# Kernel optimization log

Measured on AMD Instinct MI355X. Metric: run time of the kernel, lower is better.

The kernel has to match this reference:

```python
import jax, jax.numpy as jnp
import numpy as np

N = 200000          # number of points (dental scan vertices)
K = 16              # neighbors after dropping self (nsample=17 - 1)
C = 32              # feature dim (base_fdim)
NUM_CLASSES = 17
TEMPERATURE = 0.1
WEIGHT = 0.1        # head_cfg.weight[1:] of '.1'
EPS = 1e-8


def setup_inputs() -> dict:
    key = jax.random.key(0)
    k1, k2, k3 = jax.random.split(key, 3)
    features = jax.random.normal(k1, (N, C), dtype=jnp.float32)
    labels = jax.random.randint(k2, (N,), 0, NUM_CLASSES, dtype=jnp.int32)
    neighbor_idx = jax.random.randint(k3, (N, K), 0, N, dtype=jnp.int64)
    return {"features": features, "labels": labels, "neighbor_idx": neighbor_idx}


def reference(features, labels, neighbor_idx):
    # gather neighbor features/labels: [N, K, C] / [N, K]
    nb_feat = features[neighbor_idx]
    nb_lab = labels[neighbor_idx]

    # posmask_cnt: same class as center point (labels are argmaxed one-hots)
    posmask = nb_lab == labels[:, None]                     # [N, K] bool

    # point_mask: points with at least one positive and one negative neighbor
    cnt = jnp.sum(posmask.astype(jnp.int32), axis=-1)       # [N]
    point_mask = jnp.logical_and(cnt > 0, cnt < K)          # [N] bool

    # dist_l2
    diff = features[:, None, :] - nb_feat                   # [N, K, C]
    dist = jnp.sqrt(jnp.sum(diff * diff, axis=-1) + EPS)    # [N, K]

    # contrast_softnn (stable softmax over neighbors)
    d = -dist
    d = (d - jnp.max(d, axis=-1, keepdims=True)) / TEMPERATURE
    e = jnp.exp(d)                                          # [N, K]
    pos = jnp.sum(e * posmask.astype(e.dtype), axis=-1)
    neg = jnp.sum(e, axis=-1)
    loss = -jnp.log(pos / neg + EPS)                        # [N]

    # masked mean over valid points (== filtering before the mean)
    pm = point_mask.astype(loss.dtype)
    denom = jnp.maximum(jnp.sum(pm), 1.0)
    mean_loss = jnp.sum(loss * pm) / denom
    return mean_loss * WEIGHT
```

## Files before the change

kernel.cpp:

```cpp
#include <hip/hip_runtime.h>
#include <math.h>
#include <string.h>

#define NPTS 200000
#define KNBR 16
#define CDIM 32
#define NITEM (NPTS * KNBR)
#define TEMP 0.1f
#define WEIGHT 0.1f
#define EPSV 1e-8f

#define PART_BLOCKS 2048
#define CHUNK (NITEM / 1024)
#define BLD_BLOCKS ((NPTS + 255) / 256)

#define SMP_BLOCKS 625
#define SMP_STRIDE (SMP_BLOCKS * 256)
#define SMP_ITER (NITEM / SMP_STRIDE)

#define QS 0.55f

#define TBLA_OFF 256
#define TBLB_OFF (TBLA_OFF + NPTS * 16)
#define D2A_OFF  (TBLB_OFF + NPTS * 16)
#define D2B_OFF  (D2A_OFF + NITEM * 2)
#define BL_OFF   (D2B_OFF + NITEM * 2)
#define BC_OFF   (BL_OFF + SMP_BLOCKS * 4)
#define WS_NEEDED ((size_t)(BC_OFF + SMP_BLOCKS * 4))

typedef float v2f __attribute__((ext_vector_type(2)));

static __device__ __forceinline__ unsigned short f32_to_f16b(float x) {
    _Float16 h = (_Float16)x;
    unsigned short u;
    __builtin_memcpy(&u, &h, 2);
    return u;
}
static __device__ __forceinline__ float f16b_to_f32(unsigned short u) {
    _Float16 h;
    __builtin_memcpy(&h, &u, 2);
    return (float)h;
}
static __device__ __forceinline__ int q4(float x) {
    int q = (int)rintf(x * (1.0f / QS)) + 7;
    return q < 0 ? 0 : (q > 14 ? 14 : q);
}

__global__ __launch_bounds__(256) void build_tables(
    const float* __restrict__ f, const int* __restrict__ labels,
    unsigned char* __restrict__ A, unsigned char* __restrict__ B) {
    const int p = blockIdx.x * 256 + threadIdx.x;
    if (p >= NPTS) return;
    const float4* fp = (const float4*)(f + (size_t)p * CDIM);
    const float4 v0 = fp[0], v1 = fp[1], v2 = fp[2], v3 = fp[3];
    const float4 v4 = fp[4], v5 = fp[5], v6 = fp[6], v7 = fp[7];

    int a0 = 0, a1 = 0, a2 = 0, a3 = 0;
    a0 = __builtin_amdgcn_cvt_pk_fp8_f32(v0.x, v0.y, a0, false);
    a0 = __builtin_amdgcn_cvt_pk_fp8_f32(v0.z, v0.w, a0, true);
    a1 = __builtin_amdgcn_cvt_pk_fp8_f32(v1.x, v1.y, a1, false);
    a1 = __builtin_amdgcn_cvt_pk_fp8_f32(v1.z, v1.w, a1, true);
    a2 = __builtin_amdgcn_cvt_pk_fp8_f32(v2.x, v2.y, a2, false);
    a2 = __builtin_amdgcn_cvt_pk_fp8_f32(v2.z, v2.w, a2, true);
    a3 = __builtin_amdgcn_cvt_pk_fp8_f32(v3.x, v3.y, a3, false);
    a3 = __builtin_amdgcn_cvt_pk_fp8_f32(v3.z, v3.w, a3, true);
    uint4 ra; ra.x = a0; ra.y = a1; ra.z = a2; ra.w = a3;
    *(uint4*)(A + (size_t)p * 16) = ra;

    int b0 = 0, b1 = 0, b2 = 0, b3 = 0;
    b0 = __builtin_amdgcn_cvt_pk_fp8_f32(v4.x, v4.y, b0, false);
    b0 = __builtin_amdgcn_cvt_pk_fp8_f32(v4.z, v4.w, b0, true);
    b1 = __builtin_amdgcn_cvt_pk_fp8_f32(v5.x, v5.y, b1, false);
    b1 = __builtin_amdgcn_cvt_pk_fp8_f32(v5.z, v5.w, b1, true);
    b2 = __builtin_amdgcn_cvt_pk_fp8_f32(v6.x, v6.y, b2, false);
    b2 = __builtin_amdgcn_cvt_pk_fp8_f32(v6.z, v6.w, b2, true);
    b3 = __builtin_amdgcn_cvt_pk_fp8_f32(v7.x, v7.y, b3, false);
    const int pk = q4(v7.z) | (q4(v7.w) << 4);
    b3 = (b3 & 0xffff) | (pk << 16) | ((labels[p] & 0xff) << 24);
    uint4 rb; rb.x = b0; rb.y = b1; rb.z = b2; rb.w = b3;
    *(uint4*)(B + (size_t)p * 16) = rb;
}

__global__ __launch_bounds__(256) void partial_d2(
    const unsigned char* __restrict__ tblA,
    const unsigned char* __restrict__ tblB,
    const int* __restrict__ nbr,
    unsigned short* __restrict__ d2A,
    unsigned short* __restrict__ d2B) {
    const int b = blockIdx.x;
    const int grp = (b >> 2) & 1;
    const int r = (b >> 3) * 4 + (b & 3);
    const int i0 = r * CHUNK;

    if (grp == 0) {
        for (int t = threadIdx.x; t < CHUNK; t += 256) {
            const int i = i0 + t;
            const int idx = nbr[i];
            const int p = i >> 4;
            const uint4 nv = *(const uint4*)(tblA + (size_t)idx * 16);
            const uint4 cv = *(const uint4*)(tblA + (size_t)p * 16);
            const unsigned* pn = (const unsigned*)&nv;
            const unsigned* pc = (const unsigned*)&cv;
            float d2 = 0.f;
            #pragma unroll
            for (int q = 0; q < 4; ++q) {
                v2f nl = __builtin_amdgcn_cvt_pk_f32_fp8((int)pn[q], false);
                v2f nh = __builtin_amdgcn_cvt_pk_f32_fp8((int)pn[q], true);
                v2f cl = __builtin_amdgcn_cvt_pk_f32_fp8((int)pc[q], false);
                v2f ch = __builtin_amdgcn_cvt_pk_f32_fp8((int)pc[q], true);
                float a0 = cl.x - nl.x, a1 = cl.y - nl.y;
                float a2 = ch.x - nh.x, a3 = ch.y - nh.y;
                d2 += a0 * a0 + a1 * a1 + a2 * a2 + a3 * a3;
            }
            d2A[i] = f32_to_f16b(d2);
        }
    } else {
        for (int t = threadIdx.x; t < CHUNK; t += 256) {
            const int i = i0 + t;
            const int idx = nbr[i];
            const int p = i >> 4;
            const uint4 nv = *(const uint4*)(tblB + (size_t)idx * 16);
            const uint4 cv = *(const uint4*)(tblB + (size_t)p * 16);
            const unsigned* pn = (const unsigned*)&nv;
            const unsigned* pc = (const unsigned*)&cv;
            float d2 = 0.f;
            #pragma unroll
            for (int q = 0; q < 3; ++q) {
                v2f nl = __builtin_amdgcn_cvt_pk_f32_fp8((int)pn[q], false);
                v2f nh = __builtin_amdgcn_cvt_pk_f32_fp8((int)pn[q], true);
                v2f cl = __builtin_amdgcn_cvt_pk_f32_fp8((int)pc[q], false);
                v2f ch = __builtin_amdgcn_cvt_pk_f32_fp8((int)pc[q], true);
                float a0 = cl.x - nl.x, a1 = cl.y - nl.y;
                float a2 = ch.x - nh.x, a3 = ch.y - nh.y;
                d2 += a0 * a0 + a1 * a1 + a2 * a2 + a3 * a3;
            }
            {
                v2f nl = __builtin_amdgcn_cvt_pk_f32_fp8((int)pn[3], false);
                v2f cl = __builtin_amdgcn_cvt_pk_f32_fp8((int)pc[3], false);
                float a0 = cl.x - nl.x, a1 = cl.y - nl.y;
                d2 += a0 * a0 + a1 * a1;
            }
            {
                const unsigned nb = (pn[3] >> 16) & 0xffu;
                const unsigned cb = (pc[3] >> 16) & 0xffu;
                const float n30 = (float)(nb & 15u) * QS - 7.0f * QS;
                const float n31 = (float)(nb >> 4) * QS - 7.0f * QS;
                const float c30 = (float)(cb & 15u) * QS - 7.0f * QS;
                const float c31 = (float)(cb >> 4) * QS - 7.0f * QS;
                const float a0 = c30 - n30, a1 = c31 - n31;
                d2 += a0 * a0 + a1 * a1;
            }
            const bool pos = (pn[3] >> 24) == (pc[3] >> 24);
            d2B[i] = (unsigned short)(f32_to_f16b(d2) | (pos ? 0x8000u : 0u));
        }
    }
}

__global__ __launch_bounds__(256) void softmax_part(
    const unsigned short* __restrict__ d2A,
    const unsigned short* __restrict__ d2B,
    float* __restrict__ bl, float* __restrict__ bc) {
    const int tid = threadIdx.x;
    const int lane = tid & 63;
    float loss_acc = 0.f, valid_acc = 0.f;

    for (int k = 0; k < SMP_ITER; ++k) {
        const int i = blockIdx.x * 256 + tid + k * SMP_STRIDE;
        const unsigned short ua = d2A[i];
        const unsigned short ub = d2B[i];
        const bool pos = (ub & 0x8000u) != 0;
        const float d2v = f16b_to_f32(ua) + f16b_to_f32(ub & 0x7fffu);
        const float d = sqrtf(d2v + EPSV);

        float mn = d;
        mn = fminf(mn, __shfl_xor(mn, 1));
        mn = fminf(mn, __shfl_xor(mn, 2));
        mn = fminf(mn, __shfl_xor(mn, 4));
        mn = fminf(mn, __shfl_xor(mn, 8));
        const float e = expf((mn - d) * (1.0f / TEMP));

        float pos_s = pos ? e : 0.f;
        float neg_s = e;
        float cnt_s = pos ? 1.f : 0.f;
        #pragma unroll
        for (int off = 1; off <= 8; off <<= 1) {
            pos_s += __shfl_xor(pos_s, off);
            neg_s += __shfl_xor(neg_s, off);
            cnt_s += __shfl_xor(cnt_s, off);
        }
        if ((lane & 15) == 0) {
            const int icnt = (int)(cnt_s + 0.5f);
            if (icnt > 0 && icnt < KNBR) {
                loss_acc += -logf(pos_s / neg_s + EPSV);
                valid_acc += 1.f;
            }
        }
    }

    loss_acc += __shfl_xor(loss_acc, 16);
    valid_acc += __shfl_xor(valid_acc, 16);
    loss_acc += __shfl_xor(loss_acc, 32);
    valid_acc += __shfl_xor(valid_acc, 32);

    __shared__ float sl[4], sv[4];
    if (lane == 0) { sl[tid >> 6] = loss_acc; sv[tid >> 6] = valid_acc; }
    __syncthreads();
    if (tid == 0) {
        bl[blockIdx.x] = sl[0] + sl[1] + sl[2] + sl[3];
        bc[blockIdx.x] = sv[0] + sv[1] + sv[2] + sv[3];
    }
}

__global__ __launch_bounds__(256) void final_reduce(const float* __restrict__ bl,
                                                    const float* __restrict__ bc,
                                                    float* __restrict__ out) {
    const int tid = threadIdx.x;
    float l = 0.f, v = 0.f;
    for (int i = tid; i < SMP_BLOCKS; i += 256) { l += bl[i]; v += bc[i]; }
    #pragma unroll
    for (int off = 1; off <= 32; off <<= 1) {
        l += __shfl_xor(l, off);
        v += __shfl_xor(v, off);
    }
    __shared__ float sl[4], sv[4];
    if ((tid & 63) == 0) { sl[tid >> 6] = l; sv[tid >> 6] = v; }
    __syncthreads();
    if (tid == 0) {
        const float S = sl[0] + sl[1] + sl[2] + sl[3];
        const float C = sv[0] + sv[1] + sv[2] + sv[3];
        out[0] = S / fmaxf(C, 1.f) * WEIGHT;
    }
}

__global__ __launch_bounds__(256) void contrast_fp32(
    const float* __restrict__ features,
    const int* __restrict__ labels,
    const int* __restrict__ nbr,
    float* __restrict__ ws) {
    const int lane = threadIdx.x & 63;
    const int wave = threadIdx.x >> 6;
    const int p0 = blockIdx.x * 16 + wave * 4;
    const int m = lane >> 3;
    const int c = lane & 7;
    const int idx_l = nbr[p0 * KNBR + lane];
    const int labn_l = labels[idx_l];
    const int labc_l = labels[p0 + (lane >> 4)];
    float4 cen[4];
    #pragma unroll
    for (int pt = 0; pt < 4; ++pt)
        cen[pt] = *(const float4*)(features + (size_t)(p0 + pt) * CDIM + c * 4);
    int ridx[8];
    #pragma unroll
    for (int j = 0; j < 8; ++j) ridx[j] = __shfl(idx_l, 8 * j + m);
    float4 v[8];
    #pragma unroll
    for (int j = 0; j < 8; ++j)
        v[j] = *(const float4*)(features + (size_t)ridx[j] * CDIM + c * 4);
    float dj[8];
    #pragma unroll
    for (int j = 0; j < 8; ++j) {
        float4 ce = cen[j >> 1];
        float dx = ce.x - v[j].x, dy = ce.y - v[j].y;
        float dz = ce.z - v[j].z, dw = ce.w - v[j].w;
        float d2 = dx * dx + dy * dy + dz * dz + dw * dw;
        d2 += __shfl_xor(d2, 1);
        d2 += __shfl_xor(d2, 2);
        d2 += __shfl_xor(d2, 4);
        dj[j] = sqrtf(d2 + EPSV);
    }
    float loss_acc = 0.f, valid_acc = 0.f;
    #pragma unroll
    for (int pt = 0; pt < 4; ++pt) {
        float a = dj[2 * pt], b = dj[2 * pt + 1];
        float mn = fminf(a, b);
        mn = fminf(mn, __shfl_xor(mn, 8));
        mn = fminf(mn, __shfl_xor(mn, 16));
        mn = fminf(mn, __shfl_xor(mn, 32));
        const float ea = expf((mn - a) / TEMP);
        const float eb = expf((mn - b) / TEMP);
        const int la = __shfl(labn_l, 16 * pt + m);
        const int lb = __shfl(labn_l, 16 * pt + 8 + m);
        const int lc = __shfl(labc_l, 16 * pt);
        float pos_s = (la == lc ? ea : 0.f) + (lb == lc ? eb : 0.f);
        float neg_s = ea + eb;
        float cnt_s = (la == lc ? 1.f : 0.f) + (lb == lc ? 1.f : 0.f);
        #pragma unroll
        for (int off = 8; off <= 32; off <<= 1) {
            pos_s += __shfl_xor(pos_s, off);
            neg_s += __shfl_xor(neg_s, off);
            cnt_s += __shfl_xor(cnt_s, off);
        }
        if (lane == pt) {
            const int icnt = (int)(cnt_s + 0.5f);
            if (icnt > 0 && icnt < KNBR) {
                loss_acc += -logf(pos_s / neg_s + EPSV);
                valid_acc += 1.f;
            }
        }
    }
    __shared__ float s_loss, s_cnt;
    if (threadIdx.x == 0) { s_loss = 0.f; s_cnt = 0.f; }
    __syncthreads();
    if (lane < 4) { atomicAdd(&s_loss, loss_acc); atomicAdd(&s_cnt, valid_acc); }
    __syncthreads();
    if (threadIdx.x == 0) { atomicAdd(&ws[0], s_loss); atomicAdd(&ws[1], s_cnt); }
}

__global__ void contrast_finalize(const float* __restrict__ ws,
                                  float* __restrict__ out) {
    out[0] = ws[0] / fmaxf(ws[1], 1.f) * WEIGHT;
}

extern "C" void kernel_launch(void* const* d_in, const int* in_sizes, int n_in,
                              void* d_out, int out_size, void* d_ws, size_t ws_size,
                              hipStream_t stream) {
    const float* features = (const float*)d_in[0];
    const int* labels     = (const int*)d_in[1];
    const int* nbr        = (const int*)d_in[2];
    float* out = (float*)d_out;
    float* ws  = (float*)d_ws;

    if (ws_size >= WS_NEEDED) {
        unsigned char* tblA = (unsigned char*)d_ws + TBLA_OFF;
        unsigned char* tblB = (unsigned char*)d_ws + TBLB_OFF;
        unsigned short* d2A = (unsigned short*)((char*)d_ws + D2A_OFF);
        unsigned short* d2B = (unsigned short*)((char*)d_ws + D2B_OFF);
        float* bl = (float*)((char*)d_ws + BL_OFF);
        float* bc = (float*)((char*)d_ws + BC_OFF);

        build_tables<<<BLD_BLOCKS, 256, 0, stream>>>(features, labels, tblA, tblB);
        partial_d2<<<PART_BLOCKS, 256, 0, stream>>>(tblA, tblB, nbr, d2A, d2B);
        softmax_part<<<SMP_BLOCKS, 256, 0, stream>>>(d2A, d2B, bl, bc);
        final_reduce<<<1, 256, 0, stream>>>(bl, bc, out);
    } else {
        hipMemsetAsync(ws, 0, 16, stream);
        contrast_fp32<<<NPTS / 16, 256, 0, stream>>>(features, labels, nbr, ws);
        contrast_finalize<<<1, 1, 0, stream>>>(ws, out);
    }
}
```

Baseline: 138.0 us.

## Process four neighbors per thread with vectorized loads and nontemporal hints

The pairwise-distance kernel now gives each thread four consecutive neighbor entries of one point. It loads the four indices as one vector, loads and decodes the center row once, and stores the four fp16 results as a single 8-byte nontemporal write. The softmax kernel likewise reads four entries per thread, cutting the per-point shuffle reductions from 16 lanes to 4. Nontemporal loads are added for the streamed feature, index and intermediate buffers. This trades lower load instruction count, fewer shuffles and less redundant center decoding for more registers per thread and a grid-stride loop in place of fixed chunks.

```diff
diff --git a/kernel.cpp b/kernel.cpp
--- a/kernel.cpp
+++ b/kernel.cpp
@@ -10,13 +10,15 @@
 #define WEIGHT 0.1f
 #define EPSV 1e-8f
 
-#define PART_BLOCKS 2048
-#define CHUNK (NITEM / 1024)
 #define BLD_BLOCKS ((NPTS + 255) / 256)
 
+#define PD_BLOCKS 1248
+#define PD_RANKS 3125
+#define PD_GSTRIDE 624
+
 #define SMP_BLOCKS 625
-#define SMP_STRIDE (SMP_BLOCKS * 256)
-#define SMP_ITER (NITEM / SMP_STRIDE)
+#define SMP_ITER 5
+#define SMP_STRIDE (SMP_BLOCKS * 1024)
 
 #define QS 0.55f
 
@@ -29,6 +31,10 @@
 #define WS_NEEDED ((size_t)(BC_OFF + SMP_BLOCKS * 4))
 
 typedef float v2f __attribute__((ext_vector_type(2)));
+typedef float v4f __attribute__((ext_vector_type(4)));
+typedef int   v4i __attribute__((ext_vector_type(4)));
+typedef unsigned v4u __attribute__((ext_vector_type(4)));
+typedef unsigned v2u __attribute__((ext_vector_type(2)));
 
 static __device__ __forceinline__ unsigned short f32_to_f16b(float x) {
     _Float16 h = (_Float16)x;
@@ -51,9 +57,15 @@
     unsigned char* __restrict__ A, unsigned char* __restrict__ B) {
     const int p = blockIdx.x * 256 + threadIdx.x;
     if (p >= NPTS) return;
-    const float4* fp = (const float4*)(f + (size_t)p * CDIM);
-    const float4 v0 = fp[0], v1 = fp[1], v2 = fp[2], v3 = fp[3];
-    const float4 v4 = fp[4], v5 = fp[5], v6 = fp[6], v7 = fp[7];
+    const v4f* fp = (const v4f*)(f + (size_t)p * CDIM);
+    const v4f v0 = __builtin_nontemporal_load(fp + 0);
+    const v4f v1 = __builtin_nontemporal_load(fp + 1);
+    const v4f v2 = __builtin_nontemporal_load(fp + 2);
+    const v4f v3 = __builtin_nontemporal_load(fp + 3);
+    const v4f v4 = __builtin_nontemporal_load(fp + 4);
+    const v4f v5 = __builtin_nontemporal_load(fp + 5);
+    const v4f v6 = __builtin_nontemporal_load(fp + 6);
+    const v4f v7 = __builtin_nontemporal_load(fp + 7);
 
     int a0 = 0, a1 = 0, a2 = 0, a3 = 0;
     a0 = __builtin_amdgcn_cvt_pk_fp8_f32(v0.x, v0.y, a0, false);
@@ -64,8 +76,9 @@
     a2 = __builtin_amdgcn_cvt_pk_fp8_f32(v2.z, v2.w, a2, true);
     a3 = __builtin_amdgcn_cvt_pk_fp8_f32(v3.x, v3.y, a3, false);
     a3 = __builtin_amdgcn_cvt_pk_fp8_f32(v3.z, v3.w, a3, true);
-    uint4 ra; ra.x = a0; ra.y = a1; ra.z = a2; ra.w = a3;
-    *(uint4*)(A + (size_t)p * 16) = ra;
+    v4u ra; ra.x = (unsigned)a0; ra.y = (unsigned)a1;
+    ra.z = (unsigned)a2; ra.w = (unsigned)a3;
+    *(v4u*)(A + (size_t)p * 16) = ra;
 
     int b0 = 0, b1 = 0, b2 = 0, b3 = 0;
     b0 = __builtin_amdgcn_cvt_pk_fp8_f32(v4.x, v4.y, b0, false);
@@ -77,8 +90,9 @@
     b3 = __builtin_amdgcn_cvt_pk_fp8_f32(v7.x, v7.y, b3, false);
     const int pk = q4(v7.z) | (q4(v7.w) << 4);
     b3 = (b3 & 0xffff) | (pk << 16) | ((labels[p] & 0xff) << 24);
-    uint4 rb; rb.x = b0; rb.y = b1; rb.z = b2; rb.w = b3;
-    *(uint4*)(B + (size_t)p * 16) = rb;
+    v4u rb; rb.x = (unsigned)b0; rb.y = (unsigned)b1;
+    rb.z = (unsigned)b2; rb.w = (unsigned)b3;
+    *(v4u*)(B + (size_t)p * 16) = rb;
 }
 
 __global__ __launch_bounds__(256) void partial_d2(
@@ -90,69 +104,85 @@
     const int b = blockIdx.x;
     const int grp = (b >> 2) & 1;
     const int r = (b >> 3) * 4 + (b & 3);
-    const int i0 = r * CHUNK;
-
-    if (grp == 0) {
-        for (int t = threadIdx.x; t < CHUNK; t += 256) {
-            const int i = i0 + t;
-            const int idx = nbr[i];
-            const int p = i >> 4;
-            const uint4 nv = *(const uint4*)(tblA + (size_t)idx * 16);
-            const uint4 cv = *(const uint4*)(tblA + (size_t)p * 16);
-            const unsigned* pn = (const unsigned*)&nv;
-            const unsigned* pc = (const unsigned*)&cv;
-            float d2 = 0.f;
+    const unsigned char* __restrict__ tbl = grp ? tblB : tblA;
+    unsigned short* __restrict__ dst = grp ? d2B : d2A;
+
+    for (int rr = r; rr < PD_RANKS; rr += PD_GSTRIDE) {
+        const int i = rr * 1024 + threadIdx.x * 4;
+        const v4i idx4 = __builtin_nontemporal_load((const v4i*)(nbr + i));
+        const int p = i >> 4;
+        const v4u cv = *(const v4u*)(tbl + (size_t)p * 16);
+
+        v4u nv[4];
+        nv[0] = *(const v4u*)(tbl + (size_t)idx4.x * 16);
+        nv[1] = *(const v4u*)(tbl + (size_t)idx4.y * 16);
+        nv[2] = *(const v4u*)(tbl + (size_t)idx4.z * 16);
+        nv[3] = *(const v4u*)(tbl + (size_t)idx4.w * 16);
+
+        unsigned short o[4];
+        if (grp == 0) {
+            v2f c[8];
             #pragma unroll
             for (int q = 0; q < 4; ++q) {
-                v2f nl = __builtin_amdgcn_cvt_pk_f32_fp8((int)pn[q], false);
-                v2f nh = __builtin_amdgcn_cvt_pk_f32_fp8((int)pn[q], true);
-                v2f cl = __builtin_amdgcn_cvt_pk_f32_fp8((int)pc[q], false);
-                v2f ch = __builtin_amdgcn_cvt_pk_f32_fp8((int)pc[q], true);
-                float a0 = cl.x - nl.x, a1 = cl.y - nl.y;
-                float a2 = ch.x - nh.x, a3 = ch.y - nh.y;
-                d2 += a0 * a0 + a1 * a1 + a2 * a2 + a3 * a3;
-            }
-            d2A[i] = f32_to_f16b(d2);
-        }
-    } else {
-        for (int t = threadIdx.x; t < CHUNK; t += 256) {
-            const int i = i0 + t;
-            const int idx = nbr[i];
-            const int p = i >> 4;
-            const uint4 nv = *(const uint4*)(tblB + (size_t)idx * 16);
-            const uint4 cv = *(const uint4*)(tblB + (size_t)p * 16);
-            const unsigned* pn = (const unsigned*)&nv;
-            const unsigned* pc = (const unsigned*)&cv;
-            float d2 = 0.f;
+                c[2 * q]     = __builtin_amdgcn_cvt_pk_f32_fp8((int)cv[q], false);
+                c[2 * q + 1] = __builtin_amdgcn_cvt_pk_f32_fp8((int)cv[q], true);
+            }
+            #pragma unroll
+            for (int k = 0; k < 4; ++k) {
+                float d2 = 0.f;
+                #pragma unroll
+                for (int q = 0; q < 4; ++q) {
+                    v2f nl = __builtin_amdgcn_cvt_pk_f32_fp8((int)nv[k][q], false);
+                    v2f nh = __builtin_amdgcn_cvt_pk_f32_fp8((int)nv[k][q], true);
+                    float a0 = c[2 * q].x - nl.x, a1 = c[2 * q].y - nl.y;
+                    float a2 = c[2 * q + 1].x - nh.x, a3 = c[2 * q + 1].y - nh.y;
+                    d2 += a0 * a0 + a1 * a1 + a2 * a2 + a3 * a3;
+                }
+                o[k] = f32_to_f16b(d2);
+            }
+        } else {
+            v2f c[7];
             #pragma unroll
             for (int q = 0; q < 3; ++q) {
-                v2f nl = __builtin_amdgcn_cvt_pk_f32_fp8((int)pn[q], false);
-                v2f nh = __builtin_amdgcn_cvt_pk_f32_fp8((int)pn[q], true);
-                v2f cl = __builtin_amdgcn_cvt_pk_f32_fp8((int)pc[q], false);
-                v2f ch = __builtin_amdgcn_cvt_pk_f32_fp8((int)pc[q], true);
-                float a0 = cl.x - nl.x, a1 = cl.y - nl.y;
-                float a2 = ch.x - nh.x, a3 = ch.y - nh.y;
-                d2 += a0 * a0 + a1 * a1 + a2 * a2 + a3 * a3;
-            }
-            {
-                v2f nl = __builtin_amdgcn_cvt_pk_f32_fp8((int)pn[3], false);
-                v2f cl = __builtin_amdgcn_cvt_pk_f32_fp8((int)pc[3], false);
-                float a0 = cl.x - nl.x, a1 = cl.y - nl.y;
-                d2 += a0 * a0 + a1 * a1;
-            }
-            {
-                const unsigned nb = (pn[3] >> 16) & 0xffu;
-                const unsigned cb = (pc[3] >> 16) & 0xffu;
-                const float n30 = (float)(nb & 15u) * QS - 7.0f * QS;
-                const float n31 = (float)(nb >> 4) * QS - 7.0f * QS;
-                const float c30 = (float)(cb & 15u) * QS - 7.0f * QS;
-                const float c31 = (float)(cb >> 4) * QS - 7.0f * QS;
-                const float a0 = c30 - n30, a1 = c31 - n31;
-                d2 += a0 * a0 + a1 * a1;
-            }
-            const bool pos = (pn[3] >> 24) == (pc[3] >> 24);
-            d2B[i] = (unsigned short)(f32_to_f16b(d2) | (pos ? 0x8000u : 0u));
-        }
+                c[2 * q]     = __builtin_amdgcn_cvt_pk_f32_fp8((int)cv[q], false);
+                c[2 * q + 1] = __builtin_amdgcn_cvt_pk_f32_fp8((int)cv[q], true);
+            }
+            c[6] = __builtin_amdgcn_cvt_pk_f32_fp8((int)cv[3], false);
+            const unsigned cb = (cv[3] >> 16) & 0xffu;
+            const float c30 = (float)(cb & 15u) * QS - 7.0f * QS;
+            const float c31 = (float)(cb >> 4) * QS - 7.0f * QS;
+            const unsigned clab = cv[3] >> 24;
+            #pragma unroll
+            for (int k = 0; k < 4; ++k) {
+                float d2 = 0.f;
+                #pragma unroll
+                for (int q = 0; q < 3; ++q) {
+                    v2f nl = __builtin_amdgcn_cvt_pk_f32_fp8((int)nv[k][q], false);
+                    v2f nh = __builtin_amdgcn_cvt_pk_f32_fp8((int)nv[k][q], true);
+                    float a0 = c[2 * q].x - nl.x, a1 = c[2 * q].y - nl.y;
+                    float a2 = c[2 * q + 1].x - nh.x, a3 = c[2 * q + 1].y - nh.y;
+                    d2 += a0 * a0 + a1 * a1 + a2 * a2 + a3 * a3;
+                }
+                {
+                    v2f nl = __builtin_amdgcn_cvt_pk_f32_fp8((int)nv[k][3], false);
+                    float a0 = c[6].x - nl.x, a1 = c[6].y - nl.y;
+                    d2 += a0 * a0 + a1 * a1;
+                }
+                {
+                    const unsigned nb = (nv[k][3] >> 16) & 0xffu;
+                    const float n30 = (float)(nb & 15u) * QS - 7.0f * QS;
+                    const float n31 = (float)(nb >> 4) * QS - 7.0f * QS;
+                    const float a0 = c30 - n30, a1 = c31 - n31;
+                    d2 += a0 * a0 + a1 * a1;
+                }
+                const bool pos = (nv[k][3] >> 24) == clab;
+                o[k] = (unsigned short)(f32_to_f16b(d2) | (pos ? 0x8000u : 0u));
+            }
+        }
+        v2u pk2;
+        pk2.x = (unsigned)o[0] | ((unsigned)o[1] << 16);
+        pk2.y = (unsigned)o[2] | ((unsigned)o[3] << 16);
+        __builtin_nontemporal_store(pk2, (v2u*)(dst + i));
     }
 }
 
@@ -165,30 +195,38 @@
     float loss_acc = 0.f, valid_acc = 0.f;
 
     for (int k = 0; k < SMP_ITER; ++k) {
-        const int i = blockIdx.x * 256 + tid + k * SMP_STRIDE;
-        const unsigned short ua = d2A[i];
-        const unsigned short ub = d2B[i];
-        const bool pos = (ub & 0x8000u) != 0;
-        const float d2v = f16b_to_f32(ua) + f16b_to_f32(ub & 0x7fffu);
-        const float d = sqrtf(d2v + EPSV);
-
-        float mn = d;
+        const int i = blockIdx.x * 1024 + tid * 4 + k * SMP_STRIDE;
+        const v2u ua = __builtin_nontemporal_load((const v2u*)(d2A + i));
+        const v2u ub = __builtin_nontemporal_load((const v2u*)(d2B + i));
+
+        float d[4];
+        bool pos[4];
+        #pragma unroll
+        for (int j = 0; j < 4; ++j) {
+            const unsigned short a = (unsigned short)((j < 2 ? ua.x : ua.y) >> ((j & 1) * 16));
+            const unsigned short bb = (unsigned short)((j < 2 ? ub.x : ub.y) >> ((j & 1) * 16));
+            pos[j] = (bb & 0x8000u) != 0;
+            d[j] = sqrtf(f16b_to_f32(a) + f16b_to_f32(bb & 0x7fffu) + EPSV);
+        }
+
+        float mn = fminf(fminf(d[0], d[1]), fminf(d[2], d[3]));
         mn = fminf(mn, __shfl_xor(mn, 1));
         mn = fminf(mn, __shfl_xor(mn, 2));
-        mn = fminf(mn, __shfl_xor(mn, 4));
-        mn = fminf(mn, __shfl_xor(mn, 8));
-        const float e = expf((mn - d) * (1.0f / TEMP));
-
-        float pos_s = pos ? e : 0.f;
-        float neg_s = e;
-        float cnt_s = pos ? 1.f : 0.f;
+
+        float pos_s = 0.f, neg_s = 0.f, cnt_s = 0.f;
         #pragma unroll
-        for (int off = 1; off <= 8; off <<= 1) {
+        for (int j = 0; j < 4; ++j) {
+            const float e = expf((mn - d[j]) * (1.0f / TEMP));
+            neg_s += e;
+            if (pos[j]) { pos_s += e; cnt_s += 1.f; }
+        }
+        #pragma unroll
+        for (int off = 1; off <= 2; off <<= 1) {
             pos_s += __shfl_xor(pos_s, off);
             neg_s += __shfl_xor(neg_s, off);
             cnt_s += __shfl_xor(cnt_s, off);
         }
-        if ((lane & 15) == 0) {
+        if ((lane & 3) == 0) {
             const int icnt = (int)(cnt_s + 0.5f);
             if (icnt > 0 && icnt < KNBR) {
                 loss_acc += -logf(pos_s / neg_s + EPSV);
@@ -197,10 +235,11 @@
         }
     }
 
-    loss_acc += __shfl_xor(loss_acc, 16);
-    valid_acc += __shfl_xor(valid_acc, 16);
-    loss_acc += __shfl_xor(loss_acc, 32);
-    valid_acc += __shfl_xor(valid_acc, 32);
+    #pragma unroll
+    for (int off = 4; off <= 32; off <<= 1) {
+        loss_acc += __shfl_xor(loss_acc, off);
+        valid_acc += __shfl_xor(valid_acc, off);
+    }
 
     __shared__ float sl[4], sv[4];
     if (lane == 0) { sl[tid >> 6] = loss_acc; sv[tid >> 6] = valid_acc; }
@@ -329,11 +368,11 @@
         float* bc = (float*)((char*)d_ws + BC_OFF);
 
         build_tables<<<BLD_BLOCKS, 256, 0, stream>>>(features, labels, tblA, tblB);
-        partial_d2<<<PART_BLOCKS, 256, 0, stream>>>(tblA, tblB, nbr, d2A, d2B);
+        partial_d2<<<PD_BLOCKS, 256, 0, stream>>>(tblA, tblB, nbr, d2A, d2B);
         softmax_part<<<SMP_BLOCKS, 256, 0, stream>>>(d2A, d2B, bl, bc);
         final_reduce<<<1, 256, 0, stream>>>(bl, bc, out);
     } else {
-        hipMemsetAsync(ws, 0, 16, stream);
+        (void)hipMemsetAsync(ws, 0, 16, stream);
         contrast_fp32<<<NPTS / 16, 256, 0, stream>>>(features, labels, nbr, ws);
         contrast_finalize<<<1, 1, 0, stream>>>(ws, out);
     }
```

New measurement: 135.9 us, median of 2. No clear change (-1.6%).
